# Kernel tuning notes

Measured on AMD Instinct MI355X. Metric: run time of the kernel, lower is better.

Reference implementation:

```python
import jax, jax.numpy as jnp
import numpy as np

N, L, K, Dc, Db, Dd, C = 4096, 32, 8, 64, 64, 16, 8
B, M = 32, 1000  # M_samples hardcoded to 1000 in the original forward
LOG2PI = float(np.log(2.0 * np.pi))


def setup_inputs() -> dict:
    key = jax.random.key(0)
    ks = jax.random.split(key, 16)
    X_c = jax.random.normal(ks[0], (B, Dc), dtype=jnp.float32)
    X_b = (jax.random.uniform(ks[1], (B, Db)) < 0.5).astype(jnp.float32)
    X_d = jax.random.randint(ks[2], (B, Dd), 0, C, dtype=jnp.int32)
    # variational / posterior parameters (as in __init__)
    q_z_mean = jax.random.uniform(ks[3], (N, L), dtype=jnp.float32)
    q_log_var = jax.random.uniform(ks[4], (N, L), dtype=jnp.float32)
    g = jax.random.uniform(ks[5], (N, K), dtype=jnp.float32) + 1e-3
    q_s_param = g / jnp.sum(g, axis=-1, keepdims=True)  # Dirichlet-like rows
    posterior_mean = jnp.zeros((N, L), dtype=jnp.float32)
    posterior_var = jnp.ones((N, L), dtype=jnp.float32)
    posterior_mu = jnp.ones((N, K), dtype=jnp.float32) / K
    # heterogeneous FA likelihood params (per component k)
    s = 1.0 / np.sqrt(L)
    W_g = jax.random.normal(ks[6], (K, Dc, L), dtype=jnp.float32) * s
    b_g = jax.random.normal(ks[7], (K, Dc), dtype=jnp.float32) * 0.1
    logvar_g = jax.random.normal(ks[8], (K, Dc), dtype=jnp.float32) * 0.1
    W_b = jax.random.normal(ks[9], (K, Db, L), dtype=jnp.float32) * s
    b_b = jax.random.normal(ks[10], (K, Db), dtype=jnp.float32) * 0.1
    W_d = jax.random.normal(ks[11], (K, Dd, C, L), dtype=jnp.float32) * s
    b_d = jax.random.normal(ks[12], (K, Dd, C), dtype=jnp.float32) * 0.1
    eps = jax.random.normal(ks[13], (B, M, L), dtype=jnp.float32)  # rsample noise
    return dict(index=0, X_c=X_c, X_b=X_b, X_d=X_d,
                q_z_mean=q_z_mean, q_log_var=q_log_var, q_s_param=q_s_param,
                posterior_mean=posterior_mean, posterior_var=posterior_var,
                posterior_mu=posterior_mu,
                W_g=W_g, b_g=b_g, logvar_g=logvar_g,
                W_b=W_b, b_b=b_b, W_d=W_d, b_d=b_d, eps=eps)


def _log_liks(z, X_c, X_b, X_d, W_g, b_g, logvar_g, W_b, b_b, W_d, b_d):
    # z: [B,M,L] -> each term [B,K,M] (log_pdf summed over feature dims)
    mean = jnp.einsum('kdl,bml->bkmd', W_g, z) + b_g[None, :, None, :]
    var = jnp.exp(logvar_g)[None, :, None, :]
    t1 = -0.5 * jnp.sum(LOG2PI + logvar_g[None, :, None, :]
                        + (X_c[:, None, None, :] - mean) ** 2 / var, axis=-1)
    logits_b = jnp.einsum('kdl,bml->bkmd', W_b, z) + b_b[None, :, None, :]
    t2 = jnp.sum(X_b[:, None, None, :] * logits_b - jax.nn.softplus(logits_b), axis=-1)
    logits_d = jnp.einsum('kdcl,bml->bkmdc', W_d, z) + b_d[None, :, None, :, :]
    logp = jax.nn.log_softmax(logits_d, axis=-1)  # [B,K,M,Dd,C]
    idx = jnp.broadcast_to(X_d[:, None, None, :, None].astype(jnp.int32),
                           logp.shape[:-1] + (1,))
    t3 = jnp.sum(jnp.take_along_axis(logp, idx, axis=-1)[..., 0], axis=-1)
    return t1, t2, t3


def reference(index, X_c, X_b, X_d, q_z_mean, q_log_var, q_s_param,
              posterior_mean, posterior_var, posterior_mu,
              W_g, b_g, logvar_g, W_b, b_b, W_d, b_d, eps):
    start = B * index
    end = start + B
    qm = q_z_mean[start:end]        # [B,L]
    qlv = q_log_var[start:end]      # [B,L]
    qs = q_s_param[start:end]       # [B,K]
    mp = posterior_mean[start:end]
    vp = posterior_var[start:end]
    pmu = posterior_mu[start:end]
    # reparameterized MC samples z ~ q_z
    z = qm[:, None, :] + jnp.exp(0.5 * qlv)[:, None, :] * eps  # [B,M,L]
    t1, t2, t3 = _log_liks(z, X_c, X_b, X_d, W_g, b_g, logvar_g, W_b, b_b, W_d, b_d)
    # LL_i = sum_k q_s[i,k] * sum_m (t1+t2+t3)  (sum, no /M, as in original)
    LL = jnp.sum(qs * jnp.sum(t1 + t2 + t3, axis=-1))
    # KL(q_z || p_z), both diagonal MVNs
    vq = jnp.exp(qlv)
    klz = 0.5 * jnp.sum(jnp.log(vp) - qlv + (vq + (qm - mp) ** 2) / vp - 1.0, axis=-1)
    # KL(q_s || p_s), Categorical normalizes probs
    qn = qs / jnp.sum(qs, axis=-1, keepdims=True)
    pn = pmu / jnp.sum(pmu, axis=-1, keepdims=True)
    kls = jnp.sum(qn * (jnp.log(qn) - jnp.log(pn)), axis=-1)
    elbo = LL - jnp.sum(klz) - jnp.sum(kls)
    KL_z = klz[-1]   # original returns last iteration's KL
    KL_s = kls[-1]
    term_1 = jnp.sum(t1, axis=(0, 1))  # [M]
    term_2 = jnp.sum(t2, axis=(0, 1))
    term_3 = jnp.sum(t3, axis=(0, 1))
    rik = jnp.zeros((N, K), dtype=jnp.float32).at[start:end].set(
        jax.nn.softmax(qs, axis=-1))
    rik = jax.lax.stop_gradient(rik)
    return (-elbo, LL, KL_z, KL_s, rik, term_1, term_2, term_3)
```

## Files before the change

### kernel.cpp

```cpp
#include <hip/hip_runtime.h>
#include <math.h>

#define N_ 4096
#define L_ 32
#define K_ 8
#define Dc_ 64
#define Db_ 64
#define Dd_ 16
#define C_ 8
#define B_ 32
#define M_ 1000
#define LOG2PI_ 1.8378770664093453f

#define OUT_RIK 4
#define OUT_T1 (4 + N_ * K_)

#define WS_PART 0
#define WS_LLP  98304
#define WS_WP   99328
#define WS_BIAS (WS_WP + 32768)
#define WS_IV   (WS_BIAS + 2048)
#define WS_C1   (WS_IV + 512)

typedef __attribute__((ext_vector_type(8))) short short8v;
typedef __attribute__((ext_vector_type(4))) float f32x4;

__device__ inline unsigned short f2bf(float f) {
    unsigned u = __builtin_bit_cast(unsigned, f);
    unsigned r = u + 0x7FFFu + ((u >> 16) & 1u);
    return (unsigned short)(r >> 16);
}

#define PW  65536
#define PB  (PW + 2048)
#define PIV (PB + 512)
#define PC1 (PIV + 9)

__global__ __launch_bounds__(256) void mm_prep(
    const float* __restrict__ Wg, const float* __restrict__ bg, const float* __restrict__ lvg,
    const float* __restrict__ Wb, const float* __restrict__ bb,
    const float* __restrict__ Wd, const float* __restrict__ bd,
    float* __restrict__ ws)
{
    const int t = blockIdx.x * 256 + threadIdx.x;
    unsigned short* wpw = (unsigned short*)(ws + WS_WP);

    if (t < PW) {
        int j = t & 7, lane = (t >> 3) & 63, ft = (t >> 9) & 15, k = t >> 13;
        int f = ft * 16 + (lane & 15);
        int l = (lane >> 4) * 8 + j;
        float w;
        if (f < 64)       w = Wg[((size_t)k * 64 + f) * L_ + l];
        else if (f < 128) w = Wb[((size_t)k * 64 + (f - 64)) * L_ + l];
        else { int d = (f - 128) >> 3, c = f & 7; w = Wd[(((size_t)k * 16 + d) * 8 + c) * L_ + l]; }
        wpw[t] = f2bf(w);
    } else if (t < PB) {
        int i = t - PW; int k = i >> 8, f = i & 255;
        float v;
        if (f < 64)       v = bg[k * 64 + f];
        else if (f < 128) v = bb[k * 64 + f - 64];
        else { int d = (f - 128) >> 3, c = f & 7; v = bd[(k * 16 + d) * 8 + c]; }
        ws[WS_BIAS + i] = v;
    } else if (t < PIV) {
        int i = t - PB;
        ws[WS_IV + i] = __expf(-lvg[i]);
    } else if (t < PC1) {
        int k = t - PIV;
        if (k < 8) {
            float s = 0.f;
            for (int d = 0; d < 64; ++d) s += LOG2PI_ + lvg[k * 64 + d];
            ws[WS_C1 + k] = s;
        } else {
            float s = 0.f;
            for (int i = 0; i < 512; ++i) s += LOG2PI_ + lvg[i];
            ws[WS_C1 + 8] = s;
        }
    }
}

__global__ __launch_bounds__(512, 2) void mm_main(
    const int* __restrict__ pidx,
    const float* __restrict__ Xc, const float* __restrict__ Xb, const int* __restrict__ Xd,
    const float* __restrict__ qm_all, const float* __restrict__ qlv_all,
    const float* __restrict__ qs_all, const float* __restrict__ eps,
    float* __restrict__ ws)
{
    const int tid = threadIdx.x, w = tid >> 6, lane = tid & 63;
    const int mt = blockIdx.x, b = blockIdx.y;
    const int l15 = lane & 15, lg = lane >> 4;
    const int fr = 4 * lg;
    const int start = B_ * pidx[0];
    const unsigned short* wp = (const unsigned short*)(ws + WS_WP);

    __shared__ __align__(16) unsigned int zu[1024];
    __shared__ __align__(16) float scin[2048];
    __shared__ __align__(16) float siv[512];
    __shared__ float sqk[8];
    __shared__ float sred[8][4][2][16];
    __shared__ float llred[8];

    {
        int m_loc = tid >> 3, l0 = (tid & 7) * 4;
        int m_glob = mt * 64 + m_loc;
        float4 e = make_float4(0.f, 0.f, 0.f, 0.f);
        if (m_glob < M_) e = *(const float4*)(eps + ((size_t)b * M_ + m_glob) * L_ + l0);
        float4 qm4 = *(const float4*)(qm_all + (size_t)(start + b) * L_ + l0);
        float4 ql4 = *(const float4*)(qlv_all + (size_t)(start + b) * L_ + l0);
        float z0 = qm4.x + __expf(0.5f * ql4.x) * e.x;
        float z1 = qm4.y + __expf(0.5f * ql4.y) * e.y;
        float z2 = qm4.z + __expf(0.5f * ql4.z) * e.z;
        float z3 = qm4.w + __expf(0.5f * ql4.w) * e.w;
        unsigned u0 = (unsigned)f2bf(z0) | ((unsigned)f2bf(z1) << 16);
        unsigned u1 = (unsigned)f2bf(z2) | ((unsigned)f2bf(z3) << 16);
        int widx = (m_loc >> 4) * 256 + ((l0 >> 3) * 16 + (m_loc & 15)) * 4 + ((l0 & 7) >> 1);
        zu[widx] = u0; zu[widx + 1] = u1;
    }
    {
        int f = (tid & 63) * 4;
        float4 bv = *(const float4*)(ws + WS_BIAS + tid * 4);
        if (f < 64) {
            float4 xc = *(const float4*)(Xc + b * 64 + f);
            bv.x -= xc.x; bv.y -= xc.y; bv.z -= xc.z; bv.w -= xc.w;
        }
        ((float4*)scin)[tid] = bv;
    }
    if (tid < 128) ((float4*)siv)[tid] = *(const float4*)(ws + WS_IV + tid * 4);
    if (tid < 8)   sqk[tid] = qs_all[(size_t)(start + b) * K_ + tid];
    __syncthreads();

    const unsigned short* zp = (const unsigned short*)zu;
    const short8v zbA = *(const short8v*)(zp + lane * 8);
    const short8v zbB = *(const short8v*)(zp + 512 + lane * 8);
    const short8v zbC = *(const short8v*)(zp + 1024 + lane * 8);
    const short8v zbD = *(const short8v*)(zp + 1536 + lane * 8);

    const float4 xf = *(const float4*)(Xb + b * 64 + (w & 3) * 16 + fr);
    const int d3 = 2 * w + (lg >> 1);
    const int xd = Xd[b * 16 + d3];
    const int cc0 = 4 * (lg & 1);
    float4 is3;
    is3.x = (cc0 + 0 == xd) ? 1.f : 0.f;  is3.y = (cc0 + 1 == xd) ? 1.f : 0.f;
    is3.z = (cc0 + 2 == xd) ? 1.f : 0.f;  is3.w = (cc0 + 3 == xd) ? 1.f : 0.f;

    float taA = 0.f, taB = 0.f, taC = 0.f, taD = 0.f;
    float tbA = 0.f, tbB = 0.f, tbC = 0.f, tbD = 0.f;
    float llA = 0.f, llB = 0.f, llC = 0.f, llD = 0.f;

#define GAUSS_EPI(dd, ta_, ll_) { \
    float s_ = 0.f; \
    s_ = fmaf(dd[0] * dd[0], iv4.x, s_); \
    s_ = fmaf(dd[1] * dd[1], iv4.y, s_); \
    s_ = fmaf(dd[2] * dd[2], iv4.z, s_); \
    s_ = fmaf(dd[3] * dd[3], iv4.w, s_); \
    ta_ += s_; ll_ = fmaf(qm5, s_, ll_); }

#define BERN_EPI(dd, ta_, ll_) { \
    float s_ = 0.f, lgt_, sp_; \
    lgt_ = dd[0]; sp_ = fmaxf(lgt_, 0.f) + __logf(1.f + __expf(-fabsf(lgt_))); s_ += xf.x * lgt_ - sp_; \
    lgt_ = dd[1]; sp_ = fmaxf(lgt_, 0.f) + __logf(1.f + __expf(-fabsf(lgt_))); s_ += xf.y * lgt_ - sp_; \
    lgt_ = dd[2]; sp_ = fmaxf(lgt_, 0.f) + __logf(1.f + __expf(-fabsf(lgt_))); s_ += xf.z * lgt_ - sp_; \
    lgt_ = dd[3]; sp_ = fmaxf(lgt_, 0.f) + __logf(1.f + __expf(-fabsf(lgt_))); s_ += xf.w * lgt_ - sp_; \
    ta_ += s_; ll_ = fmaf(qkv, s_, ll_); }

#define CAT_EPI(dd, tb_, ll_) { \
    float e4_ = __expf(dd[0]) + __expf(dd[1]) + __expf(dd[2]) + __expf(dd[3]); \
    float se_ = e4_ + __shfl_xor(e4_, 16, 64); \
    float u_  = is3.x * dd[0] + is3.y * dd[1] + is3.z * dd[2] + is3.w * dd[3]; \
    float tm_ = u_ - 0.5f * __logf(se_); \
    tb_ += tm_; ll_ = fmaf(qkv, tm_, ll_); }

    #pragma unroll 2
    for (int k = 0; k < K_; ++k) {
        const short8v wfA = *(const short8v*)(wp + ((size_t)(k * 16 + w))     * 512 + lane * 8);
        const short8v wfB = *(const short8v*)(wp + ((size_t)(k * 16 + 8 + w)) * 512 + lane * 8);
        const float4 cA = *(const float4*)(scin + k * 256 + w * 16 + fr);
        const float4 cB = *(const float4*)(scin + k * 256 + (8 + w) * 16 + fr);
        const float qkv = sqk[k];

        const f32x4 ciA = {cA.x, cA.y, cA.z, cA.w};
        const f32x4 ciB = {cB.x, cB.y, cB.z, cB.w};
        f32x4 dA0 = __builtin_amdgcn_mfma_f32_16x16x32_bf16(wfA, zbA, ciA, 0, 0, 0);
        f32x4 dA1 = __builtin_amdgcn_mfma_f32_16x16x32_bf16(wfA, zbB, ciA, 0, 0, 0);
        f32x4 dA2 = __builtin_amdgcn_mfma_f32_16x16x32_bf16(wfA, zbC, ciA, 0, 0, 0);
        f32x4 dA3 = __builtin_amdgcn_mfma_f32_16x16x32_bf16(wfA, zbD, ciA, 0, 0, 0);
        f32x4 dB0 = __builtin_amdgcn_mfma_f32_16x16x32_bf16(wfB, zbA, ciB, 0, 0, 0);
        f32x4 dB1 = __builtin_amdgcn_mfma_f32_16x16x32_bf16(wfB, zbB, ciB, 0, 0, 0);
        f32x4 dB2 = __builtin_amdgcn_mfma_f32_16x16x32_bf16(wfB, zbC, ciB, 0, 0, 0);
        f32x4 dB3 = __builtin_amdgcn_mfma_f32_16x16x32_bf16(wfB, zbD, ciB, 0, 0, 0);

        if (w < 4) {
            const float4 iv4 = *(const float4*)(siv + k * 64 + w * 16 + fr);
            const float qm5 = -0.5f * qkv;
            GAUSS_EPI(dA0, taA, llA)
            GAUSS_EPI(dA1, taB, llB)
            GAUSS_EPI(dA2, taC, llC)
            GAUSS_EPI(dA3, taD, llD)
        } else {
            BERN_EPI(dA0, taA, llA)
            BERN_EPI(dA1, taB, llB)
            BERN_EPI(dA2, taC, llC)
            BERN_EPI(dA3, taD, llD)
        }
        CAT_EPI(dB0, tbA, llA)
        CAT_EPI(dB1, tbB, llB)
        CAT_EPI(dB2, tbC, llC)
        CAT_EPI(dB3, tbD, llD)
    }

    const int mrow = mt * 64 + l15;
    if (mrow      >= M_) { taA = 0.f; tbA = 0.f; llA = 0.f; }
    if (mrow + 16 >= M_) { taB = 0.f; tbB = 0.f; llB = 0.f; }
    if (mrow + 32 >= M_) { taC = 0.f; tbC = 0.f; llC = 0.f; }
    if (mrow + 48 >= M_) { taD = 0.f; tbD = 0.f; llD = 0.f; }

    float tarA = taA + __shfl_xor(taA, 16, 64); tarA += __shfl_xor(tarA, 32, 64);
    float tarB = taB + __shfl_xor(taB, 16, 64); tarB += __shfl_xor(tarB, 32, 64);
    float tarC = taC + __shfl_xor(taC, 16, 64); tarC += __shfl_xor(tarC, 32, 64);
    float tarD = taD + __shfl_xor(taD, 16, 64); tarD += __shfl_xor(tarD, 32, 64);
    float tbrA = tbA + __shfl_xor(tbA, 16, 64); tbrA += __shfl_xor(tbrA, 32, 64);
    float tbrB = tbB + __shfl_xor(tbB, 16, 64); tbrB += __shfl_xor(tbrB, 32, 64);
    float tbrC = tbC + __shfl_xor(tbC, 16, 64); tbrC += __shfl_xor(tbrC, 32, 64);
    float tbrD = tbD + __shfl_xor(tbD, 16, 64); tbrD += __shfl_xor(tbrD, 32, 64);
    float llv = llA + llB + llC + llD;
    #pragma unroll
    for (int ofs = 1; ofs < 64; ofs <<= 1) llv += __shfl_xor(llv, ofs, 64);

    if (lane < 16) {
        sred[w][0][0][l15] = tarA; sred[w][1][0][l15] = tarB;
        sred[w][2][0][l15] = tarC; sred[w][3][0][l15] = tarD;
        sred[w][0][1][l15] = tbrA; sred[w][1][1][l15] = tbrB;
        sred[w][2][1][l15] = tbrC; sred[w][3][1][l15] = tbrD;
    }
    if (lane == 0) llred[w] = llv;
    __syncthreads();

    if (tid < 192) {
        int i = tid >> 6, tile = (tid >> 4) & 3, cx = tid & 15;
        int rt = mt * 4 + tile;
        float s;
        if (i == 0) {
            s = sred[0][tile][0][cx] + sred[1][tile][0][cx]
              + sred[2][tile][0][cx] + sred[3][tile][0][cx];
        } else if (i == 1) {
            s = sred[4][tile][0][cx] + sred[5][tile][0][cx]
              + sred[6][tile][0][cx] + sred[7][tile][0][cx];
        } else {
            s = 0.f;
            #pragma unroll
            for (int ww = 0; ww < 8; ++ww) s += sred[ww][tile][1][cx];
        }
        ws[WS_PART + ((size_t)b * 64 + rt) * 48 + i * 16 + cx] = s;
    }
    if (tid == 192) {
        float s = 0.f;
        #pragma unroll
        for (int ww = 0; ww < 8; ++ww) s += llred[ww];
        float cterm = 0.f;
        #pragma unroll
        for (int k = 0; k < 8; ++k) cterm = fmaf(sqk[k], ws[WS_C1 + k], cterm);
        int nv = M_ - mt * 64; nv = (nv > 64) ? 64 : (nv < 0 ? 0 : nv);
        ws[WS_LLP + b * 16 + mt] = s - 0.5f * cterm * (float)nv;
    }
}

__global__ __launch_bounds__(256) void mm_final(
    const int* __restrict__ pidx,
    const float* __restrict__ qm_all, const float* __restrict__ qlv_all,
    const float* __restrict__ qs_all,
    const float* __restrict__ pm_all, const float* __restrict__ pv_all,
    const float* __restrict__ pmu_all,
    const float* __restrict__ ws, float* __restrict__ out)
{
    const int tid = threadIdx.x;
    if (blockIdx.x == 0) {
        __shared__ float wred[4];
        __shared__ float skl[B_], sks[B_];
        const int start = B_ * pidx[0];
        float v = ws[WS_LLP + tid] + ws[WS_LLP + 256 + tid];
        #pragma unroll
        for (int ofs = 1; ofs < 64; ofs <<= 1) v += __shfl_xor(v, ofs, 64);
        if ((tid & 63) == 0) wred[tid >> 6] = v;

        if (tid < B_) {
            int r = start + tid;
            float kl = 0.f;
            for (int l = 0; l < L_; ++l) {
                float qmv = qm_all[(size_t)r * L_ + l];
                float qlv = qlv_all[(size_t)r * L_ + l];
                float mp  = pm_all[(size_t)r * L_ + l];
                float vp  = pv_all[(size_t)r * L_ + l];
                float d   = qmv - mp;
                kl += __logf(vp) - qlv + (__expf(qlv) + d * d) / vp - 1.f;
            }
            skl[tid] = 0.5f * kl;

            float qsum = 0.f, psum = 0.f;
            #pragma unroll
            for (int j = 0; j < K_; ++j) {
                qsum += qs_all[(size_t)r * K_ + j];
                psum += pmu_all[(size_t)r * K_ + j];
            }
            float ks = 0.f;
            #pragma unroll
            for (int j = 0; j < K_; ++j) {
                float qn = qs_all[(size_t)r * K_ + j] / qsum;
                float pn = pmu_all[(size_t)r * K_ + j] / psum;
                ks += qn * (__logf(qn) - __logf(pn));
            }
            sks[tid] = ks;
        }
        __syncthreads();
        if (tid == 0) {
            float LL = wred[0] + wred[1] + wred[2] + wred[3];
            float sklz = 0.f, skls = 0.f;
            for (int i = 0; i < B_; ++i) { sklz += skl[i]; skls += sks[i]; }
            float elbo = LL - sklz - skls;
            out[0] = -elbo;
            out[1] = LL;
            out[2] = skl[B_ - 1];
            out[3] = sks[B_ - 1];
        }
    } else if (blockIdx.x <= 12) {
        int g = (blockIdx.x - 1) * 256 + tid;
        if (g < 3 * M_) {
            int i = g / M_, m = g % M_;
            int rt = m >> 4, cx = m & 15;
            float s = 0.f;
            #pragma unroll 8
            for (int b2 = 0; b2 < 32; ++b2)
                s += ws[WS_PART + ((size_t)b2 * 64 + rt) * 48 + i * 16 + cx];
            if (i == 0) s = -0.5f * (32.f * ws[WS_C1 + 8] + s);
            out[OUT_T1 + i * M_ + m] = s;
        }
    } else {
        int i = (blockIdx.x - 13) * 256 + tid;
        int r = i >> 3, c = i & 7;
        int start = B_ * pidx[0];
        float v = 0.f;
        if (r >= start && r < start + B_) {
            const float* row = qs_all + (size_t)r * K_;
            float mx = row[0];
            #pragma unroll
            for (int jj = 1; jj < K_; ++jj) mx = fmaxf(mx, row[jj]);
            float se = 0.f;
            #pragma unroll
            for (int jj = 0; jj < K_; ++jj) se += __expf(row[jj] - mx);
            v = __expf(row[c] - mx) / se;
        }
        out[OUT_RIK + i] = v;
    }
}

extern "C" void kernel_launch(void* const* d_in, const int* in_sizes, int n_in,
                              void* d_out, int out_size, void* d_ws, size_t ws_size,
                              hipStream_t stream)
{
    (void)in_sizes; (void)n_in; (void)out_size; (void)ws_size;
    const int*   pidx = (const int*)d_in[0];
    const float* Xc   = (const float*)d_in[1];
    const float* Xb   = (const float*)d_in[2];
    const int*   Xd   = (const int*)d_in[3];
    const float* qm   = (const float*)d_in[4];
    const float* qlv  = (const float*)d_in[5];
    const float* qs   = (const float*)d_in[6];
    const float* pm   = (const float*)d_in[7];
    const float* pv   = (const float*)d_in[8];
    const float* pmu  = (const float*)d_in[9];
    const float* Wg   = (const float*)d_in[10];
    const float* bg   = (const float*)d_in[11];
    const float* lvg  = (const float*)d_in[12];
    const float* Wb   = (const float*)d_in[13];
    const float* bb   = (const float*)d_in[14];
    const float* Wd   = (const float*)d_in[15];
    const float* bd   = (const float*)d_in[16];
    const float* eps  = (const float*)d_in[17];
    float* out = (float*)d_out;
    float* ws  = (float*)d_ws;

    mm_prep<<<(PC1 + 255) / 256, 256, 0, stream>>>(Wg, bg, lvg, Wb, bb, Wd, bd, ws);

    dim3 grid(16, 32);
    mm_main<<<grid, 512, 0, stream>>>(pidx, Xc, Xb, Xd, qm, qlv, qs, eps, ws);

    mm_final<<<141, 256, 0, stream>>>(pidx, qm, qlv, qs, pm, pv, pmu, ws, out);
}
```

Measured before the change: 41.57 us.

## Fuse weight prep kernel into main kernel, preload bf16 weights into registers

Removes the separate mm_prep launch. Each mm_main block now reads the fp32 weights, biases and log-variances directly, converts the weights to bf16 MFMA fragments in registers for all K up front, and computes the inverse variances and per-component constants in-block. This drops one kernel launch and the workspace round trip. In exchange every block repeats the conversion and global weight reads, and keeping 16 short8v fragments live raises register pressure under launch_bounds(512,2), which could cause spills.

```diff
diff --git a/kernel.cpp b/kernel.cpp
--- a/kernel.cpp
+++ b/kernel.cpp
@@ -17,10 +17,7 @@
 
 #define WS_PART 0
 #define WS_LLP  98304
-#define WS_WP   99328
-#define WS_BIAS (WS_WP + 32768)
-#define WS_IV   (WS_BIAS + 2048)
-#define WS_C1   (WS_IV + 512)
+#define WS_C1   98816
 
 typedef __attribute__((ext_vector_type(8))) short short8v;
 typedef __attribute__((ext_vector_type(4))) float f32x4;
@@ -31,58 +28,24 @@
     return (unsigned short)(r >> 16);
 }
 
-#define PW  65536
-#define PB  (PW + 2048)
-#define PIV (PB + 512)
-#define PC1 (PIV + 9)
-
-__global__ __launch_bounds__(256) void mm_prep(
-    const float* __restrict__ Wg, const float* __restrict__ bg, const float* __restrict__ lvg,
-    const float* __restrict__ Wb, const float* __restrict__ bb,
-    const float* __restrict__ Wd, const float* __restrict__ bd,
-    float* __restrict__ ws)
-{
-    const int t = blockIdx.x * 256 + threadIdx.x;
-    unsigned short* wpw = (unsigned short*)(ws + WS_WP);
-
-    if (t < PW) {
-        int j = t & 7, lane = (t >> 3) & 63, ft = (t >> 9) & 15, k = t >> 13;
-        int f = ft * 16 + (lane & 15);
-        int l = (lane >> 4) * 8 + j;
-        float w;
-        if (f < 64)       w = Wg[((size_t)k * 64 + f) * L_ + l];
-        else if (f < 128) w = Wb[((size_t)k * 64 + (f - 64)) * L_ + l];
-        else { int d = (f - 128) >> 3, c = f & 7; w = Wd[(((size_t)k * 16 + d) * 8 + c) * L_ + l]; }
-        wpw[t] = f2bf(w);
-    } else if (t < PB) {
-        int i = t - PW; int k = i >> 8, f = i & 255;
-        float v;
-        if (f < 64)       v = bg[k * 64 + f];
-        else if (f < 128) v = bb[k * 64 + f - 64];
-        else { int d = (f - 128) >> 3, c = f & 7; v = bd[(k * 16 + d) * 8 + c]; }
-        ws[WS_BIAS + i] = v;
-    } else if (t < PIV) {
-        int i = t - PB;
-        ws[WS_IV + i] = __expf(-lvg[i]);
-    } else if (t < PC1) {
-        int k = t - PIV;
-        if (k < 8) {
-            float s = 0.f;
-            for (int d = 0; d < 64; ++d) s += LOG2PI_ + lvg[k * 64 + d];
-            ws[WS_C1 + k] = s;
-        } else {
-            float s = 0.f;
-            for (int i = 0; i < 512; ++i) s += LOG2PI_ + lvg[i];
-            ws[WS_C1 + 8] = s;
-        }
-    }
+__device__ inline short8v cvt8(float4 a, float4 b) {
+    short8v r;
+    r[0] = (short)f2bf(a.x); r[1] = (short)f2bf(a.y);
+    r[2] = (short)f2bf(a.z); r[3] = (short)f2bf(a.w);
+    r[4] = (short)f2bf(b.x); r[5] = (short)f2bf(b.y);
+    r[6] = (short)f2bf(b.z); r[7] = (short)f2bf(b.w);
+    return r;
 }
 
 __global__ __launch_bounds__(512, 2) void mm_main(
     const int* __restrict__ pidx,
     const float* __restrict__ Xc, const float* __restrict__ Xb, const int* __restrict__ Xd,
     const float* __restrict__ qm_all, const float* __restrict__ qlv_all,
-    const float* __restrict__ qs_all, const float* __restrict__ eps,
+    const float* __restrict__ qs_all,
+    const float* __restrict__ Wg, const float* __restrict__ bg, const float* __restrict__ lvg,
+    const float* __restrict__ Wb, const float* __restrict__ bb,
+    const float* __restrict__ Wd, const float* __restrict__ bd,
+    const float* __restrict__ eps,
     float* __restrict__ ws)
 {
     const int tid = threadIdx.x, w = tid >> 6, lane = tid & 63;
@@ -90,12 +53,12 @@
     const int l15 = lane & 15, lg = lane >> 4;
     const int fr = 4 * lg;
     const int start = B_ * pidx[0];
-    const unsigned short* wp = (const unsigned short*)(ws + WS_WP);
 
     __shared__ __align__(16) unsigned int zu[1024];
     __shared__ __align__(16) float scin[2048];
     __shared__ __align__(16) float siv[512];
     __shared__ float sqk[8];
+    __shared__ float sc1s[8];
     __shared__ float sred[8][4][2][16];
     __shared__ float llred[8];
 
@@ -116,23 +79,63 @@
         zu[widx] = u0; zu[widx + 1] = u1;
     }
     {
-        int f = (tid & 63) * 4;
-        float4 bv = *(const float4*)(ws + WS_BIAS + tid * 4);
+        int k = tid >> 6, f = (tid & 63) * 4;
+        float4 bv;
         if (f < 64) {
+            bv = *(const float4*)(bg + k * 64 + f);
             float4 xc = *(const float4*)(Xc + b * 64 + f);
             bv.x -= xc.x; bv.y -= xc.y; bv.z -= xc.z; bv.w -= xc.w;
+        } else if (f < 128) {
+            bv = *(const float4*)(bb + k * 64 + (f - 64));
+        } else {
+            bv = *(const float4*)(bd + k * 128 + (f - 128));
         }
         ((float4*)scin)[tid] = bv;
     }
-    if (tid < 128) ((float4*)siv)[tid] = *(const float4*)(ws + WS_IV + tid * 4);
-    if (tid < 8)   sqk[tid] = qs_all[(size_t)(start + b) * K_ + tid];
+    if (tid < 128) {
+        float4 lv4 = *(const float4*)(lvg + tid * 4);
+        float4 r;
+        r.x = __expf(-lv4.x); r.y = __expf(-lv4.y);
+        r.z = __expf(-lv4.z); r.w = __expf(-lv4.w);
+        ((float4*)siv)[tid] = r;
+        float c1p = 4.f * LOG2PI_ + lv4.x + lv4.y + lv4.z + lv4.w;
+        c1p += __shfl_xor(c1p, 1, 64);
+        c1p += __shfl_xor(c1p, 2, 64);
+        c1p += __shfl_xor(c1p, 4, 64);
+        c1p += __shfl_xor(c1p, 8, 64);
+        if ((tid & 15) == 0) sc1s[tid >> 4] = c1p;
+    }
+    if (tid < 8) sqk[tid] = qs_all[(size_t)(start + b) * K_ + tid];
     __syncthreads();
+
+    if (tid < 8) ws[WS_C1 + tid] = sc1s[tid];
+    else if (tid == 8) {
+        float s = 0.f;
+        #pragma unroll
+        for (int ww = 0; ww < 8; ++ww) s += sc1s[ww];
+        ws[WS_C1 + 8] = s;
+    }
 
     const unsigned short* zp = (const unsigned short*)zu;
     const short8v zbA = *(const short8v*)(zp + lane * 8);
     const short8v zbB = *(const short8v*)(zp + 512 + lane * 8);
     const short8v zbC = *(const short8v*)(zp + 1024 + lane * 8);
     const short8v zbD = *(const short8v*)(zp + 1536 + lane * 8);
+
+    const float* baseA = (w < 4) ? Wg : Wb;
+    const size_t offA = (size_t)((w & 3) * 16 + l15) * 32 + lg * 8;
+    const size_t offB = (size_t)(w * 16 + l15) * 32 + lg * 8;
+    short8v wA[K_], wB[K_];
+    #pragma unroll
+    for (int k = 0; k < K_; ++k) {
+        float4 a0 = *(const float4*)(baseA + k * 2048 + offA);
+        float4 a1 = *(const float4*)(baseA + k * 2048 + offA + 4);
+        float4 b0 = *(const float4*)(Wd + k * 4096 + offB);
+        float4 b1 = *(const float4*)(Wd + k * 4096 + offB + 4);
+        wA[k] = cvt8(a0, a1);
+        wB[k] = cvt8(b0, b1);
+    }
+    __builtin_amdgcn_sched_barrier(0);
 
     const float4 xf = *(const float4*)(Xb + b * 64 + (w & 3) * 16 + fr);
     const int d3 = 2 * w + (lg >> 1);
@@ -169,10 +172,10 @@
     float tm_ = u_ - 0.5f * __logf(se_); \
     tb_ += tm_; ll_ = fmaf(qkv, tm_, ll_); }
 
-    #pragma unroll 2
+    #pragma unroll
     for (int k = 0; k < K_; ++k) {
-        const short8v wfA = *(const short8v*)(wp + ((size_t)(k * 16 + w))     * 512 + lane * 8);
-        const short8v wfB = *(const short8v*)(wp + ((size_t)(k * 16 + 8 + w)) * 512 + lane * 8);
+        const short8v wfA = wA[k];
+        const short8v wfB = wB[k];
         const float4 cA = *(const float4*)(scin + k * 256 + w * 16 + fr);
         const float4 cB = *(const float4*)(scin + k * 256 + (8 + w) * 16 + fr);
         const float qkv = sqk[k];
@@ -257,7 +260,7 @@
         for (int ww = 0; ww < 8; ++ww) s += llred[ww];
         float cterm = 0.f;
         #pragma unroll
-        for (int k = 0; k < 8; ++k) cterm = fmaf(sqk[k], ws[WS_C1 + k], cterm);
+        for (int k = 0; k < 8; ++k) cterm = fmaf(sqk[k], sc1s[k], cterm);
         int nv = M_ - mt * 64; nv = (nv > 64) ? 64 : (nv < 0 ? 0 : nv);
         ws[WS_LLP + b * 16 + mt] = s - 0.5f * cterm * (float)nv;
     }
@@ -377,10 +380,9 @@
     float* out = (float*)d_out;
     float* ws  = (float*)d_ws;
 
-    mm_prep<<<(PC1 + 255) / 256, 256, 0, stream>>>(Wg, bg, lvg, Wb, bb, Wd, bd, ws);
-
     dim3 grid(16, 32);
-    mm_main<<<grid, 512, 0, stream>>>(pidx, Xc, Xb, Xd, qm, qlv, qs, eps, ws);
+    mm_main<<<grid, 512, 0, stream>>>(pidx, Xc, Xb, Xd, qm, qlv, qs,
+                                      Wg, bg, lvg, Wb, bb, Wd, bd, eps, ws);
 
     mm_final<<<141, 256, 0, stream>>>(pidx, qm, qlv, qs, pm, pv, pmu, ws, out);
 }
```

After: 51.09 us. +22.9%, slower.

## Rebalance wave epilogue work and move rik softmax into prep kernel

Applied to the files above, without the earlier changes.

Feature tiles are reassigned across waves. Waves 0-3 now handle Gaussian plus Bernoulli tiles, and waves 4-7 handle two categorical tiles each, instead of every wave doing a categorical tile alongside one other. The goal is to even out the transcendental-heavy epilogue load and cut branch divergence per wave. The partial-sum reduction indices are updated to match. The rik softmax/zero-fill output moves from the final kernel into the prep kernel, which shrinks the final launch to 13 blocks and takes that work off the critical tail.

```diff
diff --git a/kernel.cpp b/kernel.cpp
--- a/kernel.cpp
+++ b/kernel.cpp
@@ -35,12 +35,14 @@
 #define PB  (PW + 2048)
 #define PIV (PB + 512)
 #define PC1 (PIV + 9)
+#define PRK (PC1 + N_ * K_)
 
 __global__ __launch_bounds__(256) void mm_prep(
+    const int* __restrict__ pidx, const float* __restrict__ qs_all,
     const float* __restrict__ Wg, const float* __restrict__ bg, const float* __restrict__ lvg,
     const float* __restrict__ Wb, const float* __restrict__ bb,
     const float* __restrict__ Wd, const float* __restrict__ bd,
-    float* __restrict__ ws)
+    float* __restrict__ out, float* __restrict__ ws)
 {
     const int t = blockIdx.x * 256 + threadIdx.x;
     unsigned short* wpw = (unsigned short*)(ws + WS_WP);
@@ -75,6 +77,22 @@
             for (int i = 0; i < 512; ++i) s += LOG2PI_ + lvg[i];
             ws[WS_C1 + 8] = s;
         }
+    } else if (t < PRK) {
+        int i = t - PC1;
+        int r = i >> 3, c = i & 7;
+        int start = B_ * pidx[0];
+        float v = 0.f;
+        if (r >= start && r < start + B_) {
+            const float* row = qs_all + (size_t)r * K_;
+            float mx = row[0];
+            #pragma unroll
+            for (int jj = 1; jj < K_; ++jj) mx = fmaxf(mx, row[jj]);
+            float se = 0.f;
+            #pragma unroll
+            for (int jj = 0; jj < K_; ++jj) se += __expf(row[jj] - mx);
+            v = __expf(row[c] - mx) / se;
+        }
+        out[OUT_RIK + i] = v;
     }
 }
 
@@ -134,13 +152,21 @@
     const short8v zbC = *(const short8v*)(zp + 1024 + lane * 8);
     const short8v zbD = *(const short8v*)(zp + 1536 + lane * 8);
 
-    const float4 xf = *(const float4*)(Xb + b * 64 + (w & 3) * 16 + fr);
-    const int d3 = 2 * w + (lg >> 1);
-    const int xd = Xd[b * 16 + d3];
+    const int u = w & 3;
+    const int ftA = (w < 4) ? w : (8 + 2 * u);
+    const int ftB = (w < 4) ? (4 + w) : (9 + 2 * u);
+
+    const float4 xf = *(const float4*)(Xb + b * 64 + u * 16 + fr);
+    const int dA = 4 * u + (lg >> 1);
+    const int dB = 4 * u + 2 + (lg >> 1);
+    const int xdA = Xd[b * 16 + dA];
+    const int xdB = Xd[b * 16 + dB];
     const int cc0 = 4 * (lg & 1);
-    float4 is3;
-    is3.x = (cc0 + 0 == xd) ? 1.f : 0.f;  is3.y = (cc0 + 1 == xd) ? 1.f : 0.f;
-    is3.z = (cc0 + 2 == xd) ? 1.f : 0.f;  is3.w = (cc0 + 3 == xd) ? 1.f : 0.f;
+    float4 is3A, is3B;
+    is3A.x = (cc0 + 0 == xdA) ? 1.f : 0.f;  is3A.y = (cc0 + 1 == xdA) ? 1.f : 0.f;
+    is3A.z = (cc0 + 2 == xdA) ? 1.f : 0.f;  is3A.w = (cc0 + 3 == xdA) ? 1.f : 0.f;
+    is3B.x = (cc0 + 0 == xdB) ? 1.f : 0.f;  is3B.y = (cc0 + 1 == xdB) ? 1.f : 0.f;
+    is3B.z = (cc0 + 2 == xdB) ? 1.f : 0.f;  is3B.w = (cc0 + 3 == xdB) ? 1.f : 0.f;
 
     float taA = 0.f, taB = 0.f, taC = 0.f, taD = 0.f;
     float tbA = 0.f, tbB = 0.f, tbC = 0.f, tbD = 0.f;
@@ -154,27 +180,27 @@
     s_ = fmaf(dd[3] * dd[3], iv4.w, s_); \
     ta_ += s_; ll_ = fmaf(qm5, s_, ll_); }
 
-#define BERN_EPI(dd, ta_, ll_) { \
+#define BERN_EPI(dd, tb_, ll_) { \
     float s_ = 0.f, lgt_, sp_; \
     lgt_ = dd[0]; sp_ = fmaxf(lgt_, 0.f) + __logf(1.f + __expf(-fabsf(lgt_))); s_ += xf.x * lgt_ - sp_; \
     lgt_ = dd[1]; sp_ = fmaxf(lgt_, 0.f) + __logf(1.f + __expf(-fabsf(lgt_))); s_ += xf.y * lgt_ - sp_; \
     lgt_ = dd[2]; sp_ = fmaxf(lgt_, 0.f) + __logf(1.f + __expf(-fabsf(lgt_))); s_ += xf.z * lgt_ - sp_; \
     lgt_ = dd[3]; sp_ = fmaxf(lgt_, 0.f) + __logf(1.f + __expf(-fabsf(lgt_))); s_ += xf.w * lgt_ - sp_; \
-    ta_ += s_; ll_ = fmaf(qkv, s_, ll_); }
-
-#define CAT_EPI(dd, tb_, ll_) { \
+    tb_ += s_; ll_ = fmaf(qkv, s_, ll_); }
+
+#define CAT_EPI(dd, is_, tb_, ll_) { \
     float e4_ = __expf(dd[0]) + __expf(dd[1]) + __expf(dd[2]) + __expf(dd[3]); \
     float se_ = e4_ + __shfl_xor(e4_, 16, 64); \
-    float u_  = is3.x * dd[0] + is3.y * dd[1] + is3.z * dd[2] + is3.w * dd[3]; \
+    float u_  = is_.x * dd[0] + is_.y * dd[1] + is_.z * dd[2] + is_.w * dd[3]; \
     float tm_ = u_ - 0.5f * __logf(se_); \
     tb_ += tm_; ll_ = fmaf(qkv, tm_, ll_); }
 
     #pragma unroll 2
     for (int k = 0; k < K_; ++k) {
-        const short8v wfA = *(const short8v*)(wp + ((size_t)(k * 16 + w))     * 512 + lane * 8);
-        const short8v wfB = *(const short8v*)(wp + ((size_t)(k * 16 + 8 + w)) * 512 + lane * 8);
-        const float4 cA = *(const float4*)(scin + k * 256 + w * 16 + fr);
-        const float4 cB = *(const float4*)(scin + k * 256 + (8 + w) * 16 + fr);
+        const short8v wfA = *(const short8v*)(wp + ((size_t)(k * 16 + ftA)) * 512 + lane * 8);
+        const short8v wfB = *(const short8v*)(wp + ((size_t)(k * 16 + ftB)) * 512 + lane * 8);
+        const float4 cA = *(const float4*)(scin + k * 256 + ftA * 16 + fr);
+        const float4 cB = *(const float4*)(scin + k * 256 + ftB * 16 + fr);
         const float qkv = sqk[k];
 
         const f32x4 ciA = {cA.x, cA.y, cA.z, cA.w};
@@ -195,16 +221,20 @@
             GAUSS_EPI(dA1, taB, llB)
             GAUSS_EPI(dA2, taC, llC)
             GAUSS_EPI(dA3, taD, llD)
+            BERN_EPI(dB0, tbA, llA)
+            BERN_EPI(dB1, tbB, llB)
+            BERN_EPI(dB2, tbC, llC)
+            BERN_EPI(dB3, tbD, llD)
         } else {
-            BERN_EPI(dA0, taA, llA)
-            BERN_EPI(dA1, taB, llB)
-            BERN_EPI(dA2, taC, llC)
-            BERN_EPI(dA3, taD, llD)
-        }
-        CAT_EPI(dB0, tbA, llA)
-        CAT_EPI(dB1, tbB, llB)
-        CAT_EPI(dB2, tbC, llC)
-        CAT_EPI(dB3, tbD, llD)
+            CAT_EPI(dA0, is3A, taA, llA)
+            CAT_EPI(dA1, is3A, taB, llB)
+            CAT_EPI(dA2, is3A, taC, llC)
+            CAT_EPI(dA3, is3A, taD, llD)
+            CAT_EPI(dB0, is3B, tbA, llA)
+            CAT_EPI(dB1, is3B, tbB, llB)
+            CAT_EPI(dB2, is3B, tbC, llC)
+            CAT_EPI(dB3, is3B, tbD, llD)
+        }
     }
 
     const int mrow = mt * 64 + l15;
@@ -242,12 +272,13 @@
             s = sred[0][tile][0][cx] + sred[1][tile][0][cx]
               + sred[2][tile][0][cx] + sred[3][tile][0][cx];
         } else if (i == 1) {
-            s = sred[4][tile][0][cx] + sred[5][tile][0][cx]
-              + sred[6][tile][0][cx] + sred[7][tile][0][cx];
+            s = sred[0][tile][1][cx] + sred[1][tile][1][cx]
+              + sred[2][tile][1][cx] + sred[3][tile][1][cx];
         } else {
             s = 0.f;
             #pragma unroll
-            for (int ww = 0; ww < 8; ++ww) s += sred[ww][tile][1][cx];
+            for (int ww = 4; ww < 8; ++ww)
+                s += sred[ww][tile][0][cx] + sred[ww][tile][1][cx];
         }
         ws[WS_PART + ((size_t)b * 64 + rt) * 48 + i * 16 + cx] = s;
     }
@@ -320,7 +351,7 @@
             out[2] = skl[B_ - 1];
             out[3] = sks[B_ - 1];
         }
-    } else if (blockIdx.x <= 12) {
+    } else {
         int g = (blockIdx.x - 1) * 256 + tid;
         if (g < 3 * M_) {
             int i = g / M_, m = g % M_;
@@ -332,22 +363,6 @@
             if (i == 0) s = -0.5f * (32.f * ws[WS_C1 + 8] + s);
             out[OUT_T1 + i * M_ + m] = s;
         }
-    } else {
-        int i = (blockIdx.x - 13) * 256 + tid;
-        int r = i >> 3, c = i & 7;
-        int start = B_ * pidx[0];
-        float v = 0.f;
-        if (r >= start && r < start + B_) {
-            const float* row = qs_all + (size_t)r * K_;
-            float mx = row[0];
-            #pragma unroll
-            for (int jj = 1; jj < K_; ++jj) mx = fmaxf(mx, row[jj]);
-            float se = 0.f;
-            #pragma unroll
-            for (int jj = 0; jj < K_; ++jj) se += __expf(row[jj] - mx);
-            v = __expf(row[c] - mx) / se;
-        }
-        out[OUT_RIK + i] = v;
     }
 }
 
@@ -377,10 +392,11 @@
     float* out = (float*)d_out;
     float* ws  = (float*)d_ws;
 
-    mm_prep<<<(PC1 + 255) / 256, 256, 0, stream>>>(Wg, bg, lvg, Wb, bb, Wd, bd, ws);
+    mm_prep<<<(PRK + 255) / 256, 256, 0, stream>>>(pidx, qs, Wg, bg, lvg,
+                                                   Wb, bb, Wd, bd, out, ws);
 
     dim3 grid(16, 32);
     mm_main<<<grid, 512, 0, stream>>>(pidx, Xc, Xb, Xd, qm, qlv, qs, eps, ws);
 
-    mm_final<<<141, 256, 0, stream>>>(pidx, qm, qlv, qs, pm, pv, pmu, ws, out);
+    mm_final<<<13, 256, 0, stream>>>(pidx, qm, qlv, qs, pm, pv, pmu, ws, out);
 }
```

New measurement: 42.95 us. +3.3%, slower.
